# Performance work log

Measured on AMD Instinct MI355X. Metric: run time of the kernel, lower is better.

## Reference

```python
import jax, jax.numpy as jnp
import numpy as np

INF = 1e10
GAMMA = 1.0
P = 10       # protos_num (classes == 10)
C_IN = 64
C_H = 256
T = 2048
B = 64
CLASSES = 10


def _softmin3(a, b, c):
    return -GAMMA * jax.nn.logsumexp(-jnp.stack([a, b, c]) / GAMMA, axis=0)


def _softdtw_cost(D):
    # D: [P, T] pairwise squared-euclidean cost; classic soft-DTW DP.
    n = D.shape[0]
    def step(carry, Dt):
        r_prev, diag = carry          # R[:, t-1] and R[-1, t-1]
        up_left = diag
        prev = jnp.asarray(INF, D.dtype)   # R[-1, t]
        cur = []
        for p in range(n):            # n = P = 10, small fixed unroll
            v = Dt[p] + _softmin3(prev, r_prev[p], up_left)
            up_left = r_prev[p]
            prev = v
            cur.append(v)
        return (jnp.stack(cur), jnp.asarray(INF, D.dtype)), None
    init = (jnp.full((n,), INF, D.dtype), jnp.asarray(0.0, D.dtype))
    (r_last, _), _ = jax.lax.scan(step, init, D.T)
    return r_last[-1]


def softdtw_align(protos, h):
    # protos [C,P], h [B,C,T] -> soft alignment A [B,P,T] = dE/dD (treated as constant, as in DTP).
    pn = jnp.sum(protos * protos, axis=0)                       # [P]
    hn = jnp.sum(h * h, axis=1)                                 # [B,T]
    D = pn[None, :, None] + hn[:, None, :] - 2.0 * jnp.einsum('cp,bct->bpt', protos, h)
    A = jax.vmap(jax.grad(_softdtw_cost))(D)
    return jax.lax.stop_gradient(A)


def setup_inputs() -> dict:
    key = jax.random.key(0)
    ks = jax.random.split(key, 13)
    def rn(k, shape, scale=1.0):
        return jax.random.normal(k, shape, jnp.float32) * scale
    return {
        'x': rn(ks[0], (B, C_IN, T)),
        'conv_w': rn(ks[1], (C_H, C_IN), 1.0 / np.sqrt(C_IN)),
        'conv_b': rn(ks[2], (C_H,), 0.02),
        'protos': rn(ks[3], (C_H, P), 0.5),
        'switch': rn(ks[4], (1, 3 * P), 0.5) + 1.0,
        'enc_w': rn(ks[5], (C_H,), 1.0 / np.sqrt(C_H)),
        'enc_b': rn(ks[6], (1,), 0.02),
        'dec_w1': rn(ks[7], (512, C_H * P), 1.0 / np.sqrt(C_H * P)),
        'dec_b1': rn(ks[8], (512,), 0.02),
        'dec_w2': rn(ks[9], (1024, 512), 1.0 / np.sqrt(512)),
        'dec_b2': rn(ks[10], (1024,), 0.02),
        'dec_w3': rn(ks[11], (CLASSES, 1024), 1.0 / np.sqrt(1024)),
        'dec_b3': rn(ks[12], (CLASSES,), 0.02),
    }


def reference(x, conv_w, conv_b, protos, switch, enc_w, enc_b,
              dec_w1, dec_b1, dec_w2, dec_b2, dec_w3, dec_b3):
    # conv1 (k=1) + relu: [B, 256, T]
    h = jax.nn.relu(jnp.einsum('oc,bct->bot', conv_w, x) + conv_b[None, :, None])
    b, c, t = h.shape
    # GTP (AVG), repeated to P columns
    out1 = jnp.repeat(jnp.mean(h, axis=2)[:, :, None], P, axis=2)
    # STP (AVG): P-1 equal segments of size s, last segment takes the remainder
    s = t // P
    head = h[:, :, :(P - 1) * s].reshape(b, c, P - 1, s).mean(axis=3)
    tail = h[:, :, (P - 1) * s:].mean(axis=2, keepdims=True)
    out2 = jnp.concatenate([head, tail], axis=2)
    # DTP (AVG): row-normalized soft-DTW alignment
    A = softdtw_align(protos, h)
    A = A / jnp.sum(A, axis=2, keepdims=True)
    out3 = jnp.einsum('bct,bpt->bcp', h, A)
    concat_out = jnp.concatenate([out1, out2, out3], axis=-1)      # [B, 256, 3P]
    # encoding(concat_out[...,i] * switch[j]) fused: 1x1 conv over outer product
    proj = jnp.einsum('bci,c->bi', concat_out, enc_w)              # [B, 3P]
    logits = proj[:, :, None] * switch[0][None, None, :] + enc_b   # [B, 3P, 3P]
    attn = jax.nn.softmax(logits, axis=-1)
    # AVG switch rule
    ind = jnp.concatenate([attn[:, :, :P].mean(2),
                           attn[:, :, P:2 * P].mean(2),
                           attn[:, :, 2 * P:].mean(2)], axis=1)    # [B, 9P]
    ind = jnp.mean(jnp.argmax(ind, axis=1).astype(jnp.float32))
    op = jnp.where(ind < 0.6, 0, jnp.where(ind < 1.6, 1, 2))
    one = jnp.stack([out1, out2, out3])[op]                        # selected branch
    ensemble = jnp.einsum('bci,bij->bcj', concat_out, attn)[:, :, None, :]
    z = one.reshape(b, -1)
    z = jax.nn.relu(z @ dec_w1.T + dec_b1)
    z = jax.nn.relu(z @ dec_w2.T + dec_b2)
    out = z @ dec_w3.T + dec_b3
    return (h, out, ensemble, one, op, attn)
```

## Files before the change

### kernel.cpp

```cpp
#include <hip/hip_runtime.h>

#define B_    64
#define CIN   64
#define CH    256
#define T_    2048
#define NP    10
#define INVLN2 1.44269504088896340736f
#define INFV  1e10f
#define FPAD  16
#define DROWS 2088
#define SDIAG 33408
#define BFPAD 16
#define BKROWS 2096

static const size_t DO_H   = 0;
static const size_t DO_OUT = 33554432;
static const size_t DO_ENS = 33555072;
static const size_t DO_ONE = 34046592;
static const size_t DO_OP  = 34210432;
static const size_t DO_ATT = 34210433;

static const size_t OFF_D2 = 0;
static const size_t OFF_RF = 2138112;
static const size_t OFF_Q  = 4276224;
static const size_t OFF_BK = 6414336;
static const size_t OFF_RS = 6548480;
static const size_t OFF_RT = 6549504;
static const size_t OFF_O1 = 6549568;
static const size_t OFF_O3 = 6565952;
static const size_t OFF_IND= 6729792;
static const size_t WS_END = 6729808;

__device__ __forceinline__ float dpp_shr1_inf(float x) {
  return __int_as_float(__builtin_amdgcn_update_dpp(
      __float_as_int(INFV), __float_as_int(x), 0x111, 0xf, 0xf, false));
}
__device__ __forceinline__ float dpp_shr1_z(float x) {
  return __int_as_float(__builtin_amdgcn_update_dpp(0, __float_as_int(x), 0x111, 0xf, 0xf, true));
}
__device__ __forceinline__ float row_prefix_sum16(float v) {
  v += __int_as_float(__builtin_amdgcn_update_dpp(0, __float_as_int(v), 0x111, 0xf, 0xf, true));
  v += __int_as_float(__builtin_amdgcn_update_dpp(0, __float_as_int(v), 0x112, 0xf, 0xf, true));
  v += __int_as_float(__builtin_amdgcn_update_dpp(0, __float_as_int(v), 0x114, 0xf, 0xf, true));
  v += __int_as_float(__builtin_amdgcn_update_dpp(0, __float_as_int(v), 0x118, 0xf, 0xf, true));
  return v;
}
__device__ __forceinline__ unsigned fkey(float f) {
  unsigned u = __float_as_uint(f);
  return (u & 0x80000000u) ? ~u : (u | 0x80000000u);
}

__global__ __launch_bounds__(256) void k1_conv(const float* __restrict__ x, const float* __restrict__ w,
                                               const float* __restrict__ bias, float* __restrict__ h,
                                               float* __restrict__ out2w) {
  const int tt = blockIdx.x, ot = blockIdx.y, b = blockIdx.z;
  const int tid = threadIdx.x;
  __shared__ float xs[64][132];
  __shared__ float wt[64][64];
  const int t0 = tt * 128, o0 = ot * 64;
  {
    const float* xb = x + ((size_t)b * CIN) * T_ + t0;
#pragma unroll
    for (int k = 0; k < 8; ++k) {
      int idx = tid + k * 256;
      int c = idx >> 5, q = idx & 31;
      float4 v = *(const float4*)(xb + (size_t)c * T_ + q * 4);
      *(float4*)(&xs[c][q * 4]) = v;
    }
#pragma unroll
    for (int k = 0; k < 4; ++k) {
      int idx = tid + k * 256;
      int o = idx >> 4, c4 = (idx & 15) * 4;
      float4 v = *(const float4*)(w + (size_t)(o0 + o) * 64 + c4);
      wt[c4 + 0][o] = v.x; wt[c4 + 1][o] = v.y; wt[c4 + 2][o] = v.z; wt[c4 + 3][o] = v.w;
    }
  }
  __syncthreads();
  const int og = tid >> 4, tg = tid & 15;
  float acc[4][8];
#pragma unroll
  for (int i = 0; i < 4; ++i)
#pragma unroll
    for (int j = 0; j < 8; ++j) acc[i][j] = 0.f;
  for (int c = 0; c < 64; ++c) {
    float a0 = wt[c][og * 4 + 0], a1 = wt[c][og * 4 + 1], a2 = wt[c][og * 4 + 2], a3 = wt[c][og * 4 + 3];
    float xv[8];
#pragma unroll
    for (int j = 0; j < 8; ++j) xv[j] = xs[c][tg * 8 + j];
#pragma unroll
    for (int j = 0; j < 8; ++j) {
      acc[0][j] += a0 * xv[j]; acc[1][j] += a1 * xv[j];
      acc[2][j] += a2 * xv[j]; acc[3][j] += a3 * xv[j];
    }
  }
  const int tb = t0 + tg * 8;
  int s_lo = tb / 204; if (s_lo > 9) s_lo = 9;
  int s_hi = (tb + 7) / 204; if (s_hi > 9) s_hi = 9;
  const int cross = (s_hi > s_lo) ? ((s_lo + 1) * 204 - tb) : 8;
  int sblock = t0 / 204; if (sblock > 9) sblock = 9;
  const bool crossB = (sblock < 9) && ((sblock + 1) * 204 < t0 + 128);

  float* hb = h + ((size_t)b * CH + o0) * T_ + t0;
#pragma unroll
  for (int i = 0; i < 4; ++i) {
    const float bv = bias[o0 + og * 4 + i];
    float vs[8];
#pragma unroll
    for (int j = 0; j < 8; ++j) vs[j] = fmaxf(acc[i][j] + bv, 0.f);
    float4 v0, v1;
    v0.x = vs[0]; v0.y = vs[1]; v0.z = vs[2]; v0.w = vs[3];
    v1.x = vs[4]; v1.y = vs[5]; v1.z = vs[6]; v1.w = vs[7];
    *(float4*)(&hb[(size_t)(og * 4 + i) * T_ + tg * 8]) = v0;
    *(float4*)(&hb[(size_t)(og * 4 + i) * T_ + tg * 8 + 4]) = v1;
    float sumA = 0.f, sumB = 0.f;
#pragma unroll
    for (int j = 0; j < 8; ++j) { if (j < cross) sumA += vs[j]; else sumB += vs[j]; }
    float cLo = ((s_lo == sblock) ? sumA : 0.f) + ((s_hi == sblock) ? sumB : 0.f);
    float cHi = ((s_lo == sblock + 1) ? sumA : 0.f) + ((s_hi == sblock + 1) ? sumB : 0.f);
    float rLo = row_prefix_sum16(cLo);
    float rHi = row_prefix_sum16(cHi);
    if (tg == 15) {
      float* o2p = out2w + ((size_t)(b * CH + o0 + og * 4 + i)) * NP;
      atomicAdd(o2p + sblock, rLo);
      if (crossB) atomicAdd(o2p + sblock + 1, rHi);
    }
  }
}

__global__ __launch_bounds__(256) void k2_d2(const float* __restrict__ h, const float* __restrict__ protos,
                                             float* __restrict__ D2g, unsigned* __restrict__ bkey) {
  const int tt = blockIdx.x, b = blockIdx.y, tid = threadIdx.x;
  __shared__ float pl[2560];
  __shared__ float pn[NP];
  __shared__ unsigned smin[272];
#pragma unroll
  for (int k = 0; k < 10; ++k) pl[tid + k * 256] = protos[tid + k * 256];
  for (int i = tid; i < 272; i += 256) smin[i] = 0xFFFFFFFFu;
  __syncthreads();
  if (tid < NP) {
    float s = 0.f;
    for (int c = 0; c < CH; ++c) { float v = pl[c * NP + tid]; s += v * v; }
    pn[tid] = s;
  }
  __syncthreads();
  const int t0 = tt * 256;
  const int t = t0 + tid;
  const float* hb = h + (size_t)b * CH * T_ + t;
  float hn = 0.f, ph[NP];
#pragma unroll
  for (int p = 0; p < NP; ++p) ph[p] = 0.f;
  for (int c = 0; c < CH; ++c) {
    float hv = hb[(size_t)c * T_];
    hn += hv * hv;
#pragma unroll
    for (int p = 0; p < NP; ++p) ph[p] += pl[c * NP + p] * hv;
  }
  float* dst = D2g + (size_t)b * SDIAG + FPAD * 16;
#pragma unroll
  for (int p = 0; p < NP; ++p) {
    float dv = (pn[p] + hn - 2.f * ph[p]) * INVLN2;
    dst[(t + p) * 16 + p] = dv;
    atomicMin(&smin[tid + p], fkey(dv));
  }
  __syncthreads();
  unsigned* bk = bkey + (size_t)b * BKROWS + BFPAD + t0;
  for (int i = tid; i < 265; i += 256) atomicMin(&bk[i], smin[i]);
}

__global__ __launch_bounds__(256) void k3b_fin(float* __restrict__ out2w, float* __restrict__ out1w,
                                               unsigned* __restrict__ bkey) {
  const int b = blockIdx.x, o = threadIdx.x;
  unsigned* bk = bkey + (size_t)b * BKROWS;
  for (int i = o; i < BKROWS; i += 256) {
    unsigned u = bk[i];
    float f = (u & 0x80000000u) ? __uint_as_float(u ^ 0x80000000u) : __uint_as_float(~u);
    ((float*)bk)[i] = f;
  }
  float* p = out2w + ((size_t)(b * CH + o)) * NP;
  float vals[NP], tot = 0.f;
#pragma unroll
  for (int s = 0; s < NP; ++s) { vals[s] = p[s]; tot += vals[s]; }
  out1w[b * CH + o] = tot * (1.f / 2048.f);
#pragma unroll
  for (int s = 0; s < 9; ++s) p[s] = vals[s] * (1.f / 204.f);
  p[9] = vals[9] * (1.f / 212.f);
}

struct DPState { float m1, e1, amP, aeP, bP; };
__device__ __forceinline__ float dp_step(DPState& s, float cD, float bv, bool isB) {
  float a_m = dpp_shr1_inf(s.m1);
  float a_e = dpp_shr1_z(s.e1);
  float c_m = s.amP - s.bP;
  float mt = fminf(fminf(a_m, s.m1), c_m);
  float e = __builtin_amdgcn_exp2f(mt - a_m) * a_e
          + __builtin_amdgcn_exp2f(mt - s.m1) * s.e1
          + __builtin_amdgcn_exp2f(mt - c_m) * s.aeP;
  float m = mt + cD;
  float y = m - __builtin_amdgcn_logf(e);
  s.amP = a_m; s.aeP = a_e; s.bP = bv;
  s.m1 = m; s.e1 = e;
  return isB ? (y - cD) : y;
}

__global__ __launch_bounds__(64) void k4_dp(const float* __restrict__ D2g, const float* __restrict__ bg,
                                            float* __restrict__ Rfg, float* __restrict__ Qg,
                                            float* __restrict__ rtotg) {
  const int b = blockIdx.x;
  const int l = threadIdx.x;
  if (l >= 32) return;
  const int grp = l >> 4, lr = l & 15;
  const bool isB = (grp != 0);
  const float* __restrict__ D2b = D2g + (size_t)b * SDIAG;
  const float* __restrict__ bb  = bg + (size_t)b * BKROWS;
  float* __restrict__ Sb = (grp == 0 ? Rfg : Qg) + (size_t)b * SDIAG;

  DPState st;
  {
    float D0, b0;
    if (grp == 0) { D0 = D2b[FPAD * 16 + lr];              b0 = bb[BFPAD + 2056 * 0]; b0 = bb[BFPAD]; b0 = bb[BFPAD + 0]; }
    else          { D0 = D2b[(FPAD + 2056) * 16 + 9 - lr]; b0 = bb[BFPAD + 2056]; }
    if (grp == 0) b0 = bb[BFPAD + 0];
    float c0 = D0 - b0;
    st.m1 = (lr == 0) ? c0 : INFV; st.e1 = 1.f;
    st.amP = INFV; st.aeP = 1.f; st.bP = b0;
    Sb[FPAD * 16 + lr] = st.m1;
  }
  float ccur[8], bcur[8], n1D[8], n1B[8];
  {
    float cD0[8], cB0[8];
    if (grp == 0) {
#pragma unroll
      for (int j = 0; j < 8; ++j) {
        cD0[j] = D2b[(FPAD + 16 + j) * 16 + lr]; cB0[j] = bb[BFPAD + 16 + j];
        n1D[j] = D2b[(FPAD + 24 + j) * 16 + lr]; n1B[j] = bb[BFPAD + 24 + j];
      }
    } else {
#pragma unroll
      for (int j = 0; j < 8; ++j) {
        cD0[j] = D2b[(FPAD + 2056 - 16 - j) * 16 + 9 - lr]; cB0[j] = bb[BFPAD + 2056 - 16 - j];
        n1D[j] = D2b[(FPAD + 2056 - 24 - j) * 16 + 9 - lr]; n1B[j] = bb[BFPAD + 2056 - 24 - j];
      }
    }
#pragma unroll
    for (int j = 0; j < 8; ++j) { ccur[j] = cD0[j] - cB0[j]; bcur[j] = cB0[j]; }
  }
#pragma unroll
  for (int d = 1; d < 16; ++d) {
    float Dv, bv;
    if (grp == 0) { Dv = D2b[(FPAD + d) * 16 + lr];            bv = bb[BFPAD + d]; }
    else          { Dv = D2b[(FPAD + 2056 - d) * 16 + 9 - lr]; bv = bb[BFPAD + 2056 - d]; }
    float stv = dp_step(st, Dv - bv, bv, isB);
    if (lr > d) { st.m1 = INFV; st.e1 = 1.f; }
    Sb[(FPAD + d) * 16 + lr] = stv;
  }
  const float* pDl; const float* pBl; int drD, drB;
  if (grp == 0) { pDl = D2b + (FPAD + 32) * 16 + lr;            pBl = bb + BFPAD + 32;        drD = 128;  drB = 8; }
  else          { pDl = D2b + (FPAD + 2056 - 32) * 16 + 9 - lr; pBl = bb + BFPAD + 2056 - 32; drD = -128; drB = -8; }
  float* pSl = Sb + (FPAD + 16) * 16 + lr;
#pragma unroll 1
  for (int d0 = 16; d0 <= 2048; d0 += 8) {
    float n2D[8], n2B[8];
    if (d0 <= 2032) {
      if (grp == 0) {
#pragma unroll
        for (int j = 0; j < 8; ++j) { n2D[j] = pDl[j * 16]; n2B[j] = pBl[j]; }
      } else {
#pragma unroll
        for (int j = 0; j < 8; ++j) { n2D[j] = pDl[-j * 16]; n2B[j] = pBl[-j]; }
      }
      pDl += drD; pBl += drB;
    }
    float cnx[8], bnx[8];
#pragma unroll
    for (int j = 0; j < 8; ++j) { cnx[j] = n1D[j] - n1B[j]; bnx[j] = n1B[j]; }
#pragma unroll
    for (int j = 0; j < 8; ++j) {
      float stv = dp_step(st, ccur[j], bcur[j], isB);
      pSl[j * 16] = stv;
    }
    pSl += 128;
#pragma unroll
    for (int j = 0; j < 8; ++j) { ccur[j] = cnx[j]; bcur[j] = bnx[j]; n1D[j] = n2D[j]; n1B[j] = n2B[j]; }
  }
  {
    float Dv, bv;
    if (grp == 0) { Dv = D2b[(FPAD + 2056) * 16 + lr]; bv = bb[BFPAD + 2056]; }
    else          { Dv = D2b[FPAD * 16 + 9 - lr];      bv = bb[BFPAD + 0]; }
    float stv = dp_step(st, Dv - bv, bv, isB);
    Sb[(FPAD + 2056) * 16 + lr] = stv;
    if (l == 9) rtotg[b] = stv;
  }
}

__global__ __launch_bounds__(256) void k5_out3(const float* __restrict__ h, const float* __restrict__ Rfg,
                                               const float* __restrict__ Qg, const float* __restrict__ rtotg,
                                               float* __restrict__ out3raw, float* __restrict__ rowsumg) {
  const int tc = blockIdx.x, b = blockIdx.y, tid = threadIdx.x;
  const int t0 = tc * 128;
  __shared__ float Rfs[2304];
  __shared__ float Qs[2304];
  __shared__ float Es[2048];
  __shared__ float rsl[272];
  const float* Rfb = Rfg + (size_t)b * SDIAG + (size_t)(FPAD + t0) * 16;
  const int qlo = 2056 - t0 - 143;
  const float* Qb = Qg + (size_t)b * SDIAG + (size_t)(FPAD + qlo) * 16;
#pragma unroll
  for (int k = 0; k < 3; ++k) {
    int i4 = tid + k * 256;
    if (i4 < 576) {
      ((float4*)Rfs)[i4] = ((const float4*)Rfb)[i4];
      ((float4*)Qs)[i4]  = ((const float4*)Qb)[i4];
    }
  }
  const float rtot = rtotg[b];
  __syncthreads();
  const int p = tid & 15, w = tid >> 4;
  float part = 0.f;
#pragma unroll
  for (int k = 0; k < 8; ++k) {
    const int i = k * 16 + w;
    float E = 0.f;
    if (p < NP) {
      float rf = Rfs[(i + p) * 16 + p];
      float q  = Qs[(143 - i - p) * 16 + (9 - p)];
      E = __builtin_amdgcn_exp2f(rtot - rf - q);
      part += E;
    }
    Es[i * 16 + p] = E;
  }
  rsl[p * 17 + w] = part;
  __syncthreads();
  if (tid < NP) {
    float s = 0.f;
#pragma unroll
    for (int w2 = 0; w2 < 16; ++w2) s += rsl[tid * 17 + w2];
    atomicAdd(&rowsumg[b * 16 + tid], s);
  }
  const int c = tid;
  const float* hb = h + ((size_t)b * CH + c) * T_ + t0;
  float acc[NP];
#pragma unroll
  for (int pp = 0; pp < NP; ++pp) acc[pp] = 0.f;
  for (int t4 = 0; t4 < 32; ++t4) {
    float4 hv = *(const float4*)(hb + t4 * 4);
    float he[4] = {hv.x, hv.y, hv.z, hv.w};
#pragma unroll
    for (int u = 0; u < 4; ++u) {
      const float* ar = &Es[(t4 * 4 + u) * 16];
#pragma unroll
      for (int pp = 0; pp < NP; ++pp) acc[pp] += he[u] * ar[pp];
    }
  }
  float* dst = out3raw + ((size_t)(b * CH + c)) * NP;
#pragma unroll
  for (int pp = 0; pp < NP; ++pp) atomicAdd(dst + pp, acc[pp]);
}

__global__ __launch_bounds__(64) void k6a_head(const float* __restrict__ out1w, const float* __restrict__ out2w,
                                               const float* __restrict__ out3raw, const float* __restrict__ rowsumg,
                                               const float* __restrict__ enc_w, const float* __restrict__ enc_b,
                                               const float* __restrict__ sw, float* __restrict__ attn_out,
                                               float* __restrict__ ind_sum) {
  const int b = blockIdx.x;
  const int lane = threadIdx.x;
  float a1 = 0.f, a2[NP], a3[NP];
#pragma unroll
  for (int p = 0; p < NP; ++p) { a2[p] = 0.f; a3[p] = 0.f; }
#pragma unroll
  for (int k = 0; k < 4; ++k) {
    const int c = lane + k * 64;
    const float ew = enc_w[c];
    a1 += out1w[b * CH + c] * ew;
    const float* o2 = out2w + ((size_t)(b * CH + c)) * NP;
    const float* o3 = out3raw + ((size_t)(b * CH + c)) * NP;
#pragma unroll
    for (int p = 0; p < NP; ++p) { a2[p] += o2[p] * ew; a3[p] += o3[p] * ew; }
  }
#pragma unroll
  for (int st = 32; st >= 1; st >>= 1) {
    a1 += __shfl_xor(a1, st);
#pragma unroll
    for (int p = 0; p < NP; ++p) { a2[p] += __shfl_xor(a2[p], st); a3[p] += __shfl_xor(a3[p], st); }
  }
  __shared__ float proj[30];
  __shared__ float indv[90];
  if (lane == 0) {
#pragma unroll
    for (int p = 0; p < NP; ++p) {
      proj[p] = a1;
      proj[10 + p] = a2[p];
      proj[20 + p] = a3[p] / rowsumg[b * 16 + p];
    }
  }
  __syncthreads();
  if (lane < 30) {
    const float pj = proj[lane];
    const float eb = enc_b[0];
    float lg[30];
    float mx = -1e30f;
#pragma unroll
    for (int j = 0; j < 30; ++j) { lg[j] = pj * sw[j] + eb; mx = fmaxf(mx, lg[j]); }
    float ssum = 0.f;
#pragma unroll
    for (int j = 0; j < 30; ++j) { lg[j] = expf(lg[j] - mx); ssum += lg[j]; }
    const float inv = 1.f / ssum;
    float m0 = 0.f, m1 = 0.f, m2 = 0.f;
#pragma unroll
    for (int j = 0; j < 30; ++j) {
      const float av = lg[j] * inv;
      attn_out[(size_t)b * 900 + lane * 30 + j] = av;
      if (j < 10) m0 += av; else if (j < 20) m1 += av; else m2 += av;
    }
    indv[lane] = m0 * 0.1f; indv[30 + lane] = m1 * 0.1f; indv[60 + lane] = m2 * 0.1f;
  }
  __syncthreads();
  if (lane == 0) {
    float best = -1e30f; int bi = 0;
    for (int k = 0; k < 90; ++k) { const float v = indv[k]; if (v > best) { best = v; bi = k; } }
    atomicAdd(ind_sum, (float)bi);
  }
}

__global__ __launch_bounds__(256) void k7b_ens(const float* __restrict__ out1w, const float* __restrict__ out2w,
                                               const float* __restrict__ out3raw, const float* __restrict__ rowsumg,
                                               const float* __restrict__ attn, float* __restrict__ ens) {
  const int b = blockIdx.x, tid = threadIdx.x;
  __shared__ float at[900];
  __shared__ float s0[30];
  __shared__ float irs[NP];
  for (int k = tid; k < 900; k += 256) at[k] = attn[(size_t)b * 900 + k];
  if (tid < NP) irs[tid] = 1.f / rowsumg[b * 16 + tid];
  __syncthreads();
  if (tid < 30) {
    float s = 0.f;
    for (int i = 0; i < 10; ++i) s += at[i * 30 + tid];
    s0[tid] = s;
  }
  __syncthreads();
  const int c = tid;
  const float o1 = out1w[b * CH + c];
  float o2[NP], o3[NP];
  const float* p2 = out2w + ((size_t)(b * CH + c)) * NP;
  const float* p3 = out3raw + ((size_t)(b * CH + c)) * NP;
#pragma unroll
  for (int p = 0; p < NP; ++p) { o2[p] = p2[p]; o3[p] = p3[p] * irs[p]; }
  float* dst = ens + ((size_t)(b * CH + c)) * 30;
#pragma unroll
  for (int j = 0; j < 30; ++j) {
    float acc = o1 * s0[j];
#pragma unroll
    for (int p = 0; p < NP; ++p) acc += o2[p] * at[(10 + p) * 30 + j] + o3[p] * at[(20 + p) * 30 + j];
    dst[j] = acc;
  }
}

__global__ __launch_bounds__(256) void k7a_one(const float* __restrict__ out1w, const float* __restrict__ out3raw,
                                               const float* __restrict__ rowsumg, const float* __restrict__ indws,
                                               float* __restrict__ oneb, float* __restrict__ op_out) {
  const int b = blockIdx.x, c = threadIdx.x;
  const float ind = indws[0] * (1.f / 64.f);
  const int op = ind < 0.6f ? 0 : (ind < 1.6f ? 1 : 2);
  if (b == 0 && c == 0) op_out[0] = (float)op;
  float* dst = oneb + ((size_t)(b * CH + c)) * NP;
  if (op == 0) {
    const float v = out1w[b * CH + c];
#pragma unroll
    for (int p = 0; p < NP; ++p) dst[p] = v;
  } else if (op == 2) {
    const float* s = out3raw + ((size_t)(b * CH + c)) * NP;
#pragma unroll
    for (int p = 0; p < NP; ++p) dst[p] = s[p] / rowsumg[b * 16 + p];
  }
}

__global__ __launch_bounds__(256) void k7c_z1(const float* __restrict__ one_, const float* __restrict__ w1,
                                              float* __restrict__ z1acc) {
  const int kt = blockIdx.x;
  const int mt = blockIdx.y;
  const int tid = threadIdx.x;
  __shared__ float os[64][65];
  __shared__ float wsl[64][65];
  const int k0 = kt * 64, m0 = mt * 64;
#pragma unroll
  for (int k = 0; k < 4; ++k) {
    int idx = tid + k * 256;
    int r = idx >> 4, q = (idx & 15) * 4;
    float4 v1 = *(const float4*)(one_ + (size_t)r * 2560 + m0 + q);
    os[r][q] = v1.x; os[r][q + 1] = v1.y; os[r][q + 2] = v1.z; os[r][q + 3] = v1.w;
    float4 v2 = *(const float4*)(w1 + (size_t)(k0 + r) * 2560 + m0 + q);
    wsl[r][q] = v2.x; wsl[r][q + 1] = v2.y; wsl[r][q + 2] = v2.z; wsl[r][q + 3] = v2.w;
  }
  __syncthreads();
  const int bg = tid >> 4, kg = tid & 15;
  float acc[4][4];
#pragma unroll
  for (int i = 0; i < 4; ++i)
#pragma unroll
    for (int j = 0; j < 4; ++j) acc[i][j] = 0.f;
  for (int m = 0; m < 64; ++m) {
    float ov[4], wv[4];
#pragma unroll
    for (int i = 0; i < 4; ++i) { ov[i] = os[bg * 4 + i][m]; wv[i] = wsl[kg * 4 + i][m]; }
#pragma unroll
    for (int i = 0; i < 4; ++i)
#pragma unroll
      for (int j = 0; j < 4; ++j) acc[i][j] += ov[i] * wv[j];
  }
#pragma unroll
  for (int i = 0; i < 4; ++i)
#pragma unroll
    for (int j = 0; j < 4; ++j)
      atomicAdd(&z1acc[(size_t)(bg * 4 + i) * 512 + k0 + kg * 4 + j], acc[i][j]);
}

__global__ __launch_bounds__(256) void k7d_z2(const float* __restrict__ z1acc, const float* __restrict__ db1,
                                              const float* __restrict__ w2, float* __restrict__ z2acc) {
  const int kt = blockIdx.x;
  const int mt = blockIdx.y;
  const int tid = threadIdx.x;
  __shared__ float os[64][65];
  __shared__ float wsl[64][65];
  const int k0 = kt * 64, m0 = mt * 64;
#pragma unroll
  for (int k = 0; k < 4; ++k) {
    int idx = tid + k * 256;
    int r = idx >> 4, q = (idx & 15) * 4;
    float4 v1 = *(const float4*)(z1acc + (size_t)r * 512 + m0 + q);
    float4 bv = *(const float4*)(db1 + m0 + q);
    os[r][q] = fmaxf(v1.x + bv.x, 0.f); os[r][q + 1] = fmaxf(v1.y + bv.y, 0.f);
    os[r][q + 2] = fmaxf(v1.z + bv.z, 0.f); os[r][q + 3] = fmaxf(v1.w + bv.w, 0.f);
    float4 v2 = *(const float4*)(w2 + (size_t)(k0 + r) * 512 + m0 + q);
    wsl[r][q] = v2.x; wsl[r][q + 1] = v2.y; wsl[r][q + 2] = v2.z; wsl[r][q + 3] = v2.w;
  }
  __syncthreads();
  const int bg = tid >> 4, kg = tid & 15;
  float acc[4][4];
#pragma unroll
  for (int i = 0; i < 4; ++i)
#pragma unroll
    for (int j = 0; j < 4; ++j) acc[i][j] = 0.f;
  for (int m = 0; m < 64; ++m) {
    float ov[4], wv[4];
#pragma unroll
    for (int i = 0; i < 4; ++i) { ov[i] = os[bg * 4 + i][m]; wv[i] = wsl[kg * 4 + i][m]; }
#pragma unroll
    for (int i = 0; i < 4; ++i)
#pragma unroll
      for (int j = 0; j < 4; ++j) acc[i][j] += ov[i] * wv[j];
  }
#pragma unroll
  for (int i = 0; i < 4; ++i)
#pragma unroll
    for (int j = 0; j < 4; ++j)
      atomicAdd(&z2acc[(size_t)(bg * 4 + i) * 1024 + k0 + kg * 4 + j], acc[i][j]);
}

__global__ __launch_bounds__(64) void k7e_out(const float* __restrict__ z2acc, const float* __restrict__ db2,
                                              const float* __restrict__ w3, const float* __restrict__ db3,
                                              float* __restrict__ outp) {
  const int b = blockIdx.x, lane = threadIdx.x;
  float acc[NP];
#pragma unroll
  for (int n = 0; n < NP; ++n) acc[n] = 0.f;
  for (int j = lane; j < 1024; j += 64) {
    float zv = z2acc[(size_t)b * 1024 + j] + db2[j];
    zv = fmaxf(zv, 0.f);
#pragma unroll
    for (int n = 0; n < NP; ++n) acc[n] += zv * w3[(size_t)n * 1024 + j];
  }
#pragma unroll
  for (int n = 0; n < NP; ++n)
#pragma unroll
    for (int st = 32; st >= 1; st >>= 1) acc[n] += __shfl_xor(acc[n], st);
  if (lane == 0) {
#pragma unroll
    for (int n = 0; n < NP; ++n) outp[b * NP + n] = acc[n] + db3[n];
  }
}

extern "C" void kernel_launch(void* const* d_in, const int* in_sizes, int n_in,
                              void* d_out, int out_size, void* d_ws, size_t ws_size,
                              hipStream_t stream) {
  (void)in_sizes; (void)n_in; (void)out_size; (void)ws_size;
  const float* x      = (const float*)d_in[0];
  const float* conv_w = (const float*)d_in[1];
  const float* conv_b = (const float*)d_in[2];
  const float* protos = (const float*)d_in[3];
  const float* sw     = (const float*)d_in[4];
  const float* enc_w  = (const float*)d_in[5];
  const float* enc_b  = (const float*)d_in[6];
  const float* dw1    = (const float*)d_in[7];
  const float* db1    = (const float*)d_in[8];
  const float* dw2    = (const float*)d_in[9];
  const float* db2    = (const float*)d_in[10];
  const float* dw3    = (const float*)d_in[11];
  const float* db3    = (const float*)d_in[12];
  float* out = (float*)d_out;
  float* ws  = (float*)d_ws;

  float* D2g     = ws + OFF_D2;
  float* Rfg     = ws + OFF_RF;
  float* Qg      = ws + OFF_Q;
  unsigned* bkey = (unsigned*)(ws + OFF_BK);
  float* z1acc   = ws + OFF_BK;
  float* z2acc   = ws + OFF_BK + 32768;
  float* rowsumg = ws + OFF_RS;
  float* rtotg   = ws + OFF_RT;
  float* out1w   = ws + OFF_O1;
  float* out3raw = ws + OFF_O3;
  float* indws   = ws + OFF_IND;
  float* h       = out + DO_H;
  float* out2w   = out + DO_ONE;

  hipMemsetAsync(ws + OFF_BK, 0xFF, (size_t)64 * BKROWS * sizeof(float), stream);
  hipMemsetAsync(ws + OFF_RS, 0, (WS_END - OFF_RS) * sizeof(float), stream);
  hipMemsetAsync(out + DO_ONE, 0, (size_t)163840 * sizeof(float), stream);

  k1_conv<<<dim3(16, 4, 64), 256, 0, stream>>>(x, conv_w, conv_b, h, out2w);
  k2_d2<<<dim3(8, 64), 256, 0, stream>>>(h, protos, D2g, bkey);
  k3b_fin<<<64, 256, 0, stream>>>(out2w, out1w, bkey);
  k4_dp<<<64, 64, 0, stream>>>(D2g, (const float*)bkey, Rfg, Qg, rtotg);
  hipMemsetAsync(z1acc, 0, (size_t)98304 * sizeof(float), stream);
  k5_out3<<<dim3(16, 64), 256, 0, stream>>>(h, Rfg, Qg, rtotg, out3raw, rowsumg);
  k6a_head<<<64, 64, 0, stream>>>(out1w, out2w, out3raw, rowsumg, enc_w, enc_b, sw,
                                  out + DO_ATT, indws);
  k7b_ens<<<64, 256, 0, stream>>>(out1w, out2w, out3raw, rowsumg, out + DO_ATT, out + DO_ENS);
  k7a_one<<<64, 256, 0, stream>>>(out1w, out3raw, rowsumg, indws, out + DO_ONE, out + DO_OP);
  k7c_z1<<<dim3(8, 40), 256, 0, stream>>>(out + DO_ONE, dw1, z1acc);
  k7d_z2<<<dim3(16, 8), 256, 0, stream>>>(z1acc, db1, dw2, z2acc);
  k7e_out<<<64, 64, 0, stream>>>(z2acc, db2, dw3, db3, out + DO_OUT);
}
```

Before: 683.5 us.

## Pack four batches per wavefront and interleave two DP chains per lane

The soft-DTW DP kernel previously used one 64-thread block per batch with only 32 active lanes, each running a single serial dependency chain. Now each wave covers four batches: all 64 lanes are active, and each lane interleaves two independent DP recurrences (batch b and b+2). This is meant to hide exp/log latency through instruction-level parallelism and fill the wave. The launch shrinks to 16 blocks, so fewer CUs are used and register pressure rises.

Result: slower. 753.5 us (+10.2%).

```diff
diff --git a/kernel.cpp b/kernel.cpp
--- a/kernel.cpp
+++ b/kernel.cpp
@@ -202,93 +202,109 @@
   return isB ? (y - cD) : y;
 }
 
-__global__ __launch_bounds__(64) void k4_dp(const float* __restrict__ D2g, const float* __restrict__ bg,
-                                            float* __restrict__ Rfg, float* __restrict__ Qg,
-                                            float* __restrict__ rtotg) {
-  const int b = blockIdx.x;
+__global__ __launch_bounds__(64, 1) void k4_dp(const float* __restrict__ D2g, const float* __restrict__ bg,
+                                               float* __restrict__ Rfg, float* __restrict__ Qg,
+                                               float* __restrict__ rtotg) {
   const int l = threadIdx.x;
-  if (l >= 32) return;
   const int grp = l >> 4, lr = l & 15;
-  const bool isB = (grp != 0);
-  const float* __restrict__ D2b = D2g + (size_t)b * SDIAG;
-  const float* __restrict__ bb  = bg + (size_t)b * BKROWS;
-  float* __restrict__ Sb = (grp == 0 ? Rfg : Qg) + (size_t)b * SDIAG;
-
-  DPState st;
+  const bool isB = (grp & 1) != 0;
+  const int elem  = isB ? (9 - lr) : lr;
+  const int dstep = isB ? -16 : 16;
+  const int bstep = isB ? -1 : 1;
+  const int ld0   = isB ? (FPAD + 2056) * 16 : FPAD * 16;
+  const int lb0   = isB ? (BFPAD + 2056) : BFPAD;
+
+  const float* pD0; const float* pD1;
+  const float* pB0; const float* pB1;
+  float* pS0; float* pS1;
+  int bat0, bat1;
   {
-    float D0, b0;
-    if (grp == 0) { D0 = D2b[FPAD * 16 + lr];              b0 = bb[BFPAD + 2056 * 0]; b0 = bb[BFPAD]; b0 = bb[BFPAD + 0]; }
-    else          { D0 = D2b[(FPAD + 2056) * 16 + 9 - lr]; b0 = bb[BFPAD + 2056]; }
-    if (grp == 0) b0 = bb[BFPAD + 0];
-    float c0 = D0 - b0;
-    st.m1 = (lr == 0) ? c0 : INFV; st.e1 = 1.f;
-    st.amP = INFV; st.aeP = 1.f; st.bP = b0;
-    Sb[FPAD * 16 + lr] = st.m1;
-  }
-  float ccur[8], bcur[8], n1D[8], n1B[8];
+    bat0 = (blockIdx.x << 2) + (grp >> 1);
+    bat1 = bat0 + 2;
+    pD0 = D2g + (size_t)bat0 * SDIAG + ld0 + elem;
+    pD1 = D2g + (size_t)bat1 * SDIAG + ld0 + elem;
+    pB0 = bg + (size_t)bat0 * BKROWS + lb0;
+    pB1 = bg + (size_t)bat1 * BKROWS + lb0;
+    float* Sbase = isB ? Qg : Rfg;
+    pS0 = Sbase + (size_t)bat0 * SDIAG + FPAD * 16 + lr;
+    pS1 = Sbase + (size_t)bat1 * SDIAG + FPAD * 16 + lr;
+  }
+  DPState stA, stB;
   {
-    float cD0[8], cB0[8];
-    if (grp == 0) {
-#pragma unroll
-      for (int j = 0; j < 8; ++j) {
-        cD0[j] = D2b[(FPAD + 16 + j) * 16 + lr]; cB0[j] = bb[BFPAD + 16 + j];
-        n1D[j] = D2b[(FPAD + 24 + j) * 16 + lr]; n1B[j] = bb[BFPAD + 24 + j];
-      }
-    } else {
-#pragma unroll
-      for (int j = 0; j < 8; ++j) {
-        cD0[j] = D2b[(FPAD + 2056 - 16 - j) * 16 + 9 - lr]; cB0[j] = bb[BFPAD + 2056 - 16 - j];
-        n1D[j] = D2b[(FPAD + 2056 - 24 - j) * 16 + 9 - lr]; n1B[j] = bb[BFPAD + 2056 - 24 - j];
-      }
-    }
-#pragma unroll
-    for (int j = 0; j < 8; ++j) { ccur[j] = cD0[j] - cB0[j]; bcur[j] = cB0[j]; }
-  }
-#pragma unroll
-  for (int d = 1; d < 16; ++d) {
-    float Dv, bv;
-    if (grp == 0) { Dv = D2b[(FPAD + d) * 16 + lr];            bv = bb[BFPAD + d]; }
-    else          { Dv = D2b[(FPAD + 2056 - d) * 16 + 9 - lr]; bv = bb[BFPAD + 2056 - d]; }
-    float stv = dp_step(st, Dv - bv, bv, isB);
-    if (lr > d) { st.m1 = INFV; st.e1 = 1.f; }
-    Sb[(FPAD + d) * 16 + lr] = stv;
-  }
-  const float* pDl; const float* pBl; int drD, drB;
-  if (grp == 0) { pDl = D2b + (FPAD + 32) * 16 + lr;            pBl = bb + BFPAD + 32;        drD = 128;  drB = 8; }
-  else          { pDl = D2b + (FPAD + 2056 - 32) * 16 + 9 - lr; pBl = bb + BFPAD + 2056 - 32; drD = -128; drB = -8; }
-  float* pSl = Sb + (FPAD + 16) * 16 + lr;
+    float D0 = pD0[0], b0 = pB0[0];
+    float D1 = pD1[0], b1 = pB1[0];
+    stA.m1 = (lr == 0) ? (D0 - b0) : INFV; stA.e1 = 1.f;
+    stA.amP = INFV; stA.aeP = 1.f; stA.bP = b0;
+    stB.m1 = (lr == 0) ? (D1 - b1) : INFV; stB.e1 = 1.f;
+    stB.amP = INFV; stB.aeP = 1.f; stB.bP = b1;
+    pS0[0] = stA.m1;
+    pS1[0] = stB.m1;
+  }
+  {
+    const float* qD0 = pD0; const float* qD1 = pD1;
+    const float* qB0 = pB0; const float* qB1 = pB1;
+#pragma unroll
+    for (int d = 1; d < 16; ++d) {
+      qD0 += dstep; qB0 += bstep; qD1 += dstep; qB1 += bstep;
+      float Dv0 = qD0[0], bv0 = qB0[0];
+      float Dv1 = qD1[0], bv1 = qB1[0];
+      float sv0 = dp_step(stA, Dv0 - bv0, bv0, isB);
+      float sv1 = dp_step(stB, Dv1 - bv1, bv1, isB);
+      if (lr > d) { stA.m1 = INFV; stA.e1 = 1.f; stB.m1 = INFV; stB.e1 = 1.f; }
+      pS0[d * 16] = sv0;
+      pS1[d * 16] = sv1;
+    }
+  }
+  float cA[8], bA[8], n1DA[8], n1BA[8];
+  float cB[8], bB[8], n1DB[8], n1BB[8];
+  {
+    const float* qD0 = pD0 + 16 * dstep; const float* qB0 = pB0 + 16 * bstep;
+    const float* qD1 = pD1 + 16 * dstep; const float* qB1 = pB1 + 16 * bstep;
+#pragma unroll
+    for (int j = 0; j < 8; ++j) {
+      float Dv0 = qD0[0], bv0 = qB0[0]; cA[j] = Dv0 - bv0; bA[j] = bv0; qD0 += dstep; qB0 += bstep;
+      float Dv1 = qD1[0], bv1 = qB1[0]; cB[j] = Dv1 - bv1; bB[j] = bv1; qD1 += dstep; qB1 += bstep;
+    }
+#pragma unroll
+    for (int j = 0; j < 8; ++j) {
+      n1DA[j] = qD0[0]; n1BA[j] = qB0[0]; qD0 += dstep; qB0 += bstep;
+      n1DB[j] = qD1[0]; n1BB[j] = qB1[0]; qD1 += dstep; qB1 += bstep;
+    }
+    pD0 = qD0; pB0 = qB0; pD1 = qD1; pB1 = qB1;
+    pS0 += 256; pS1 += 256;
+  }
 #pragma unroll 1
   for (int d0 = 16; d0 <= 2048; d0 += 8) {
-    float n2D[8], n2B[8];
+    float n2DA[8], n2BA[8], n2DB[8], n2BB[8];
     if (d0 <= 2032) {
-      if (grp == 0) {
-#pragma unroll
-        for (int j = 0; j < 8; ++j) { n2D[j] = pDl[j * 16]; n2B[j] = pBl[j]; }
-      } else {
-#pragma unroll
-        for (int j = 0; j < 8; ++j) { n2D[j] = pDl[-j * 16]; n2B[j] = pBl[-j]; }
+#pragma unroll
+      for (int j = 0; j < 8; ++j) {
+        n2DA[j] = pD0[0]; n2BA[j] = pB0[0]; pD0 += dstep; pB0 += bstep;
+        n2DB[j] = pD1[0]; n2BB[j] = pB1[0]; pD1 += dstep; pB1 += bstep;
       }
-      pDl += drD; pBl += drB;
-    }
-    float cnx[8], bnx[8];
-#pragma unroll
-    for (int j = 0; j < 8; ++j) { cnx[j] = n1D[j] - n1B[j]; bnx[j] = n1B[j]; }
+    }
 #pragma unroll
     for (int j = 0; j < 8; ++j) {
-      float stv = dp_step(st, ccur[j], bcur[j], isB);
-      pSl[j * 16] = stv;
-    }
-    pSl += 128;
-#pragma unroll
-    for (int j = 0; j < 8; ++j) { ccur[j] = cnx[j]; bcur[j] = bnx[j]; n1D[j] = n2D[j]; n1B[j] = n2B[j]; }
+      float sv0 = dp_step(stA, cA[j], bA[j], isB);
+      float sv1 = dp_step(stB, cB[j], bB[j], isB);
+      pS0[j * 16] = sv0;
+      pS1[j * 16] = sv1;
+    }
+    pS0 += 128; pS1 += 128;
+#pragma unroll
+    for (int j = 0; j < 8; ++j) {
+      cA[j] = n1DA[j] - n1BA[j]; bA[j] = n1BA[j]; n1DA[j] = n2DA[j]; n1BA[j] = n2BA[j];
+      cB[j] = n1DB[j] - n1BB[j]; bB[j] = n1BB[j]; n1DB[j] = n2DB[j]; n1BB[j] = n2BB[j];
+    }
   }
   {
-    float Dv, bv;
-    if (grp == 0) { Dv = D2b[(FPAD + 2056) * 16 + lr]; bv = bb[BFPAD + 2056]; }
-    else          { Dv = D2b[FPAD * 16 + 9 - lr];      bv = bb[BFPAD + 0]; }
-    float stv = dp_step(st, Dv - bv, bv, isB);
-    Sb[(FPAD + 2056) * 16 + lr] = stv;
-    if (l == 9) rtotg[b] = stv;
+    float Dv0 = pD0[0], bv0 = pB0[0];
+    float Dv1 = pD1[0], bv1 = pB1[0];
+    float sv0 = dp_step(stA, Dv0 - bv0, bv0, isB);
+    float sv1 = dp_step(stB, Dv1 - bv1, bv1, isB);
+    pS0[0] = sv0;
+    pS1[0] = sv1;
+    if (lr == 9 && !isB) { rtotg[bat0] = sv0; rtotg[bat1] = sv1; }
   }
 }
 
@@ -619,7 +635,7 @@
   k1_conv<<<dim3(16, 4, 64), 256, 0, stream>>>(x, conv_w, conv_b, h, out2w);
   k2_d2<<<dim3(8, 64), 256, 0, stream>>>(h, protos, D2g, bkey);
   k3b_fin<<<64, 256, 0, stream>>>(out2w, out1w, bkey);
-  k4_dp<<<64, 64, 0, stream>>>(D2g, (const float*)bkey, Rfg, Qg, rtotg);
+  k4_dp<<<16, 64, 0, stream>>>(D2g, (const float*)bkey, Rfg, Qg, rtotg);
   hipMemsetAsync(z1acc, 0, (size_t)98304 * sizeof(float), stream);
   k5_out3<<<dim3(16, 64), 256, 0, stream>>>(h, Rfg, Qg, rtotg, out3raw, rowsumg);
   k6a_head<<<64, 64, 0, stream>>>(out1w, out2w, out3raw, rowsumg, enc_w, enc_b, sw,
```

## Pack two batches per DP wave and batch the transcendentals per 8-step block

Applied to the files above, without the earlier changes.

The soft-DTW DP kernel now fills all 64 lanes of a wave with two batch items (forward and backward passes for each), launching 32 blocks instead of 64 half-idle waves. Inside the 8-step unrolled loop, the min/exponent-argument chain, the exp2 evaluations, the e recurrence and the logs are split into separate phases. This lets the independent exp2 and log instructions issue back to back instead of sitting on the serial dependency chain. The cost is fewer concurrent waves on the GPU and more live registers per lane.

After: 629.2 us. 1.09x faster.

```diff
diff --git a/kernel.cpp b/kernel.cpp
--- a/kernel.cpp
+++ b/kernel.cpp
@@ -186,109 +186,132 @@
   p[9] = vals[9] * (1.f / 212.f);
 }
 
-struct DPState { float m1, e1, amP, aeP, bP; };
-__device__ __forceinline__ float dp_step(DPState& s, float cD, float bv, bool isB) {
-  float a_m = dpp_shr1_inf(s.m1);
-  float a_e = dpp_shr1_z(s.e1);
-  float c_m = s.amP - s.bP;
-  float mt = fminf(fminf(a_m, s.m1), c_m);
-  float e = __builtin_amdgcn_exp2f(mt - a_m) * a_e
-          + __builtin_amdgcn_exp2f(mt - s.m1) * s.e1
-          + __builtin_amdgcn_exp2f(mt - c_m) * s.aeP;
-  float m = mt + cD;
-  float y = m - __builtin_amdgcn_logf(e);
-  s.amP = a_m; s.aeP = a_e; s.bP = bv;
-  s.m1 = m; s.e1 = e;
-  return isB ? (y - cD) : y;
-}
-
-__global__ __launch_bounds__(64) void k4_dp(const float* __restrict__ D2g, const float* __restrict__ bg,
-                                            float* __restrict__ Rfg, float* __restrict__ Qg,
-                                            float* __restrict__ rtotg) {
-  const int b = blockIdx.x;
+__global__ __launch_bounds__(64, 1) void k4_dp(const float* __restrict__ D2g, const float* __restrict__ bg,
+                                               float* __restrict__ Rfg, float* __restrict__ Qg,
+                                               float* __restrict__ rtotg) {
   const int l = threadIdx.x;
-  if (l >= 32) return;
   const int grp = l >> 4, lr = l & 15;
-  const bool isB = (grp != 0);
-  const float* __restrict__ D2b = D2g + (size_t)b * SDIAG;
-  const float* __restrict__ bb  = bg + (size_t)b * BKROWS;
-  float* __restrict__ Sb = (grp == 0 ? Rfg : Qg) + (size_t)b * SDIAG;
-
-  DPState st;
+  const bool isB = (grp & 1) != 0;
+  const int bat = (blockIdx.x << 1) + (grp >> 1);
+  const int elem  = isB ? (9 - lr) : lr;
+  const int dstep = isB ? -16 : 16;
+  const int bstep = isB ? -1 : 1;
+  const int ld0   = isB ? (FPAD + 2056) * 16 : FPAD * 16;
+  const int lb0   = isB ? (BFPAD + 2056) : BFPAD;
+
+  const float* pD = D2g + (size_t)bat * SDIAG + ld0 + elem;
+  const float* pB = bg + (size_t)bat * BKROWS + lb0;
+  float* pS = (isB ? Qg : Rfg) + (size_t)bat * SDIAG + FPAD * 16 + lr;
+
+  float m1, e1, amP, aeP, bP;
   {
-    float D0, b0;
-    if (grp == 0) { D0 = D2b[FPAD * 16 + lr];              b0 = bb[BFPAD + 2056 * 0]; b0 = bb[BFPAD]; b0 = bb[BFPAD + 0]; }
-    else          { D0 = D2b[(FPAD + 2056) * 16 + 9 - lr]; b0 = bb[BFPAD + 2056]; }
-    if (grp == 0) b0 = bb[BFPAD + 0];
-    float c0 = D0 - b0;
-    st.m1 = (lr == 0) ? c0 : INFV; st.e1 = 1.f;
-    st.amP = INFV; st.aeP = 1.f; st.bP = b0;
-    Sb[FPAD * 16 + lr] = st.m1;
-  }
-  float ccur[8], bcur[8], n1D[8], n1B[8];
-  {
-    float cD0[8], cB0[8];
-    if (grp == 0) {
-#pragma unroll
-      for (int j = 0; j < 8; ++j) {
-        cD0[j] = D2b[(FPAD + 16 + j) * 16 + lr]; cB0[j] = bb[BFPAD + 16 + j];
-        n1D[j] = D2b[(FPAD + 24 + j) * 16 + lr]; n1B[j] = bb[BFPAD + 24 + j];
-      }
-    } else {
-#pragma unroll
-      for (int j = 0; j < 8; ++j) {
-        cD0[j] = D2b[(FPAD + 2056 - 16 - j) * 16 + 9 - lr]; cB0[j] = bb[BFPAD + 2056 - 16 - j];
-        n1D[j] = D2b[(FPAD + 2056 - 24 - j) * 16 + 9 - lr]; n1B[j] = bb[BFPAD + 2056 - 24 - j];
-      }
-    }
-#pragma unroll
-    for (int j = 0; j < 8; ++j) { ccur[j] = cD0[j] - cB0[j]; bcur[j] = cB0[j]; }
+    float D0 = pD[0], b0 = pB[0];
+    m1 = (lr == 0) ? (D0 - b0) : INFV; e1 = 1.f;
+    amP = INFV; aeP = 1.f; bP = b0;
+    pS[0] = m1;
   }
 #pragma unroll
   for (int d = 1; d < 16; ++d) {
-    float Dv, bv;
-    if (grp == 0) { Dv = D2b[(FPAD + d) * 16 + lr];            bv = bb[BFPAD + d]; }
-    else          { Dv = D2b[(FPAD + 2056 - d) * 16 + 9 - lr]; bv = bb[BFPAD + 2056 - d]; }
-    float stv = dp_step(st, Dv - bv, bv, isB);
-    if (lr > d) { st.m1 = INFV; st.e1 = 1.f; }
-    Sb[(FPAD + d) * 16 + lr] = stv;
-  }
-  const float* pDl; const float* pBl; int drD, drB;
-  if (grp == 0) { pDl = D2b + (FPAD + 32) * 16 + lr;            pBl = bb + BFPAD + 32;        drD = 128;  drB = 8; }
-  else          { pDl = D2b + (FPAD + 2056 - 32) * 16 + 9 - lr; pBl = bb + BFPAD + 2056 - 32; drD = -128; drB = -8; }
-  float* pSl = Sb + (FPAD + 16) * 16 + lr;
+    pD += dstep; pB += bstep;
+    float Dv = pD[0], bv = pB[0];
+    float cD = Dv - bv;
+    float a_m = dpp_shr1_inf(m1);
+    float a_e = dpp_shr1_z(e1);
+    float c_m = amP - bP;
+    float mt = fminf(fminf(a_m, m1), c_m);
+    float e = __builtin_amdgcn_exp2f(mt - a_m) * a_e
+            + __builtin_amdgcn_exp2f(mt - m1) * e1
+            + __builtin_amdgcn_exp2f(mt - c_m) * aeP;
+    float mn = mt + cD;
+    float y = mn - __builtin_amdgcn_logf(e);
+    amP = a_m; aeP = a_e; bP = bv;
+    m1 = mn; e1 = e;
+    if (lr > d) { m1 = INFV; e1 = 1.f; }
+    pS[d * 16] = isB ? (y - cD) : y;
+  }
+  float cA[8], bA[8], n1D[8], n1B[8];
+#pragma unroll
+  for (int j = 0; j < 8; ++j) {
+    pD += dstep; pB += bstep;
+    float Dv = pD[0], bv = pB[0];
+    cA[j] = Dv - bv; bA[j] = bv;
+  }
+#pragma unroll
+  for (int j = 0; j < 8; ++j) {
+    pD += dstep; pB += bstep;
+    n1D[j] = pD[0]; n1B[j] = pB[0];
+  }
+  pD += dstep; pB += bstep;
+  pS += 256;
+
 #pragma unroll 1
   for (int d0 = 16; d0 <= 2048; d0 += 8) {
     float n2D[8], n2B[8];
     if (d0 <= 2032) {
-      if (grp == 0) {
-#pragma unroll
-        for (int j = 0; j < 8; ++j) { n2D[j] = pDl[j * 16]; n2B[j] = pBl[j]; }
-      } else {
-#pragma unroll
-        for (int j = 0; j < 8; ++j) { n2D[j] = pDl[-j * 16]; n2B[j] = pBl[-j]; }
+#pragma unroll
+      for (int j = 0; j < 8; ++j) {
+        n2D[j] = pD[0]; n2B[j] = pB[0];
+        pD += dstep; pB += bstep;
       }
-      pDl += drD; pBl += drB;
-    }
-    float cnx[8], bnx[8];
-#pragma unroll
-    for (int j = 0; j < 8; ++j) { cnx[j] = n1D[j] - n1B[j]; bnx[j] = n1B[j]; }
+    }
+    float g1[8], g2[8], g3[8], msv[8];
 #pragma unroll
     for (int j = 0; j < 8; ++j) {
-      float stv = dp_step(st, ccur[j], bcur[j], isB);
-      pSl[j * 16] = stv;
-    }
-    pSl += 128;
-#pragma unroll
-    for (int j = 0; j < 8; ++j) { ccur[j] = cnx[j]; bcur[j] = bnx[j]; n1D[j] = n2D[j]; n1B[j] = n2B[j]; }
+      float a_m = dpp_shr1_inf(m1);
+      float c_m = amP - bP;
+      float mt = fminf(fminf(a_m, m1), c_m);
+      g1[j] = mt - a_m; g2[j] = mt - m1; g3[j] = mt - c_m;
+      float mn = mt + cA[j];
+      amP = a_m; bP = bA[j];
+      msv[j] = mn; m1 = mn;
+    }
+    float w1[8], w2[8], w3[8];
+#pragma unroll
+    for (int j = 0; j < 8; ++j) {
+      w1[j] = __builtin_amdgcn_exp2f(g1[j]);
+      w2[j] = __builtin_amdgcn_exp2f(g2[j]);
+      w3[j] = __builtin_amdgcn_exp2f(g3[j]);
+    }
+    float esv[8];
+#pragma unroll
+    for (int j = 0; j < 8; ++j) {
+      float a_e = dpp_shr1_z(e1);
+      float t = w2[j] * e1;
+      t = fmaf(w1[j], a_e, t);
+      t = fmaf(w3[j], aeP, t);
+      aeP = a_e; e1 = t; esv[j] = t;
+    }
+    float lg[8];
+#pragma unroll
+    for (int j = 0; j < 8; ++j) lg[j] = __builtin_amdgcn_logf(esv[j]);
+#pragma unroll
+    for (int j = 0; j < 8; ++j) {
+      float y = msv[j] - lg[j];
+      y = isB ? (y - cA[j]) : y;
+      pS[j * 16] = y;
+    }
+    pS += 128;
+#pragma unroll
+    for (int j = 0; j < 8; ++j) {
+      cA[j] = n1D[j] - n1B[j]; bA[j] = n1B[j];
+      n1D[j] = n2D[j]; n1B[j] = n2B[j];
+    }
   }
   {
-    float Dv, bv;
-    if (grp == 0) { Dv = D2b[(FPAD + 2056) * 16 + lr]; bv = bb[BFPAD + 2056]; }
-    else          { Dv = D2b[FPAD * 16 + 9 - lr];      bv = bb[BFPAD + 0]; }
-    float stv = dp_step(st, Dv - bv, bv, isB);
-    Sb[(FPAD + 2056) * 16 + lr] = stv;
-    if (l == 9) rtotg[b] = stv;
+    float Dv = pD[0], bv = pB[0];
+    float cD = Dv - bv;
+    float a_m = dpp_shr1_inf(m1);
+    float a_e = dpp_shr1_z(e1);
+    float c_m = amP - bP;
+    float mt = fminf(fminf(a_m, m1), c_m);
+    float e = __builtin_amdgcn_exp2f(mt - a_m) * a_e
+            + __builtin_amdgcn_exp2f(mt - m1) * e1
+            + __builtin_amdgcn_exp2f(mt - c_m) * aeP;
+    float mn = mt + cD;
+    float y = mn - __builtin_amdgcn_logf(e);
+    float sv = isB ? (y - cD) : y;
+    pS[0] = sv;
+    if (!isB && lr == 9) rtotg[bat] = sv;
   }
 }
 
@@ -619,7 +642,7 @@
   k1_conv<<<dim3(16, 4, 64), 256, 0, stream>>>(x, conv_w, conv_b, h, out2w);
   k2_d2<<<dim3(8, 64), 256, 0, stream>>>(h, protos, D2g, bkey);
   k3b_fin<<<64, 256, 0, stream>>>(out2w, out1w, bkey);
-  k4_dp<<<64, 64, 0, stream>>>(D2g, (const float*)bkey, Rfg, Qg, rtotg);
+  k4_dp<<<32, 64, 0, stream>>>(D2g, (const float*)bkey, Rfg, Qg, rtotg);
   hipMemsetAsync(z1acc, 0, (size_t)98304 * sizeof(float), stream);
   k5_out3<<<dim3(16, 64), 256, 0, stream>>>(h, Rfg, Qg, rtotg, out3raw, rowsumg);
   k6a_head<<<64, 64, 0, stream>>>(out1w, out2w, out3raw, rowsumg, enc_w, enc_b, sw,
```
